# Kernel tuning notes

Hardware: AMD Instinct MI355X
Metric: run time of the kernel (lower is better)

## Reference

```python
import jax, jax.numpy as jnp
import numpy as np

KERNEL_MUL = 2.0
KERNEL_NUM = 5

N_S = 4096
N_T = 4096
D = 512
N_CLS = 10


def setup_inputs() -> dict:
    key = jax.random.key(0)
    k1, k2, k3 = jax.random.split(key, 3)
    x = jax.random.normal(k1, (N_S + N_T, D), dtype=jnp.float32)
    # source-first domain labels: first N_S are source (0), rest target (1)
    domain_labels = jnp.concatenate(
        [jnp.zeros((N_S,), dtype=jnp.int32), jnp.ones((N_T,), dtype=jnp.int32)]
    )
    y_true = jax.random.randint(k2, (N_S,), 0, N_CLS, dtype=jnp.int32)
    im_weights = jax.random.uniform(k3, (N_CLS,), dtype=jnp.float32, minval=0.5, maxval=1.5)
    return {
        "x": x,
        "im_weights": im_weights,
        "domain_labels": domain_labels,
        "y_true": y_true,
        "alpha": 1,
    }


def _gaussian_kernel_sum(total, n_samples):
    # Pairwise squared L2 distances via Gram trick instead of the O(N^2*D)
    # broadcasted tensor the torch code materializes (same math).
    sq = jnp.sum(total * total, axis=1)                      # [N]
    l2 = sq[:, None] + sq[None, :] - 2.0 * (total @ total.T)  # [N, N]
    l2 = jnp.maximum(l2, 0.0)
    # bandwidth computed on detached distances (torch uses L2_distance.data)
    bandwidth = jnp.sum(jax.lax.stop_gradient(l2)) / float(n_samples * n_samples - n_samples)
    bandwidth = bandwidth / (KERNEL_MUL ** (KERNEL_NUM // 2))
    k = jnp.zeros_like(l2)
    for i in range(KERNEL_NUM):
        k = k + jnp.exp(-l2 / (bandwidth * (KERNEL_MUL ** i)))
    return k


def reference(x, im_weights, domain_labels, y_true, alpha):
    dl = np.asarray(domain_labels)  # int labels are concrete constants
    src = np.where(dl == 0)[0]
    tgt = np.where(dl == 1)[0]
    n_s, n_t = len(src), len(tgt)

    total = jnp.concatenate([x[src], x[tgt]], axis=0)        # [n_s+n_t, D]
    kernels = _gaussian_kernel_sum(total, n_s + n_t)         # [N, N]

    # importance weights are detached in the torch code
    iw = jax.lax.stop_gradient(alpha * im_weights + (1.0 - alpha))
    w = iw[y_true]                                           # [n_s]

    k_ss = kernels[:n_s, :n_s]
    k_tt = kernels[n_s:, n_s:]
    k_st = kernels[:n_s, n_s:]

    # loss_1: weighted source upper-triangle + unweighted target upper-triangle
    loss_1 = jnp.sum(jnp.triu(k_ss * (w[:, None] * w[None, :]), k=1)) / float(n_s * (n_s - 1) / 2)
    loss_1 = loss_1 + jnp.sum(jnp.triu(k_tt, k=1)) / float(n_t * (n_t - 1) / 2)

    # loss_2: cross term, weighted by source sample weights
    loss_2 = jnp.sum(k_st * w[:, None]) / float(n_s * n_t)

    return loss_1 - 2.0 * loss_2
```

## Files before the change

### kernel.cpp

```cpp
#include <hip/hip_runtime.h>
#include <math.h>

#define N_TOT 8192
#define N_SRC 4096
#define D_DIM 512
#define BM2 256
#define NT2 (N_TOT / BM2)
#define NTILES2 (NT2 * (NT2 + 1) / 2)
#define NPREP 256

typedef short bf16x8 __attribute__((ext_vector_type(8)));
typedef unsigned short u16x8 __attribute__((ext_vector_type(8)));
typedef float f32x4 __attribute__((ext_vector_type(4)));


__device__ __forceinline__ unsigned short f2bf_rn(float v) {
    unsigned int u = __float_as_uint(v);
    unsigned int r = (u + 0x7FFFu + ((u >> 16) & 1u)) >> 16;
    return (unsigned short)r;
}

__global__ __launch_bounds__(256) void k_prep(const float* __restrict__ x,
                                              unsigned short* __restrict__ xhi,
                                              float* __restrict__ sq,
                                              float* __restrict__ colpart) {
    const int wave = threadIdx.x >> 6;
    const int lane = threadIdx.x & 63;
    __shared__ float colbuf[4][512];
    float fcol[8];
#pragma unroll
    for (int j = 0; j < 8; ++j) fcol[j] = 0.f;
#pragma unroll
    for (int r8 = 0; r8 < 8; ++r8) {
        const int row = blockIdx.x * 32 + wave * 8 + r8;
        const size_t base = (size_t)row * D_DIM + lane * 8;
        float v[8];
        *(float4*)&v[0] = *(const float4*)(x + base);
        *(float4*)&v[4] = *(const float4*)(x + base + 4);
        u16x8 h;
        float s = 0.f;
#pragma unroll
        for (int j = 0; j < 8; ++j) {
            h[j] = f2bf_rn(v[j]);
            s = fmaf(v[j], v[j], s);
            fcol[j] += v[j];
        }
        *(u16x8*)(xhi + base) = h;
#pragma unroll
        for (int off = 32; off; off >>= 1) s += __shfl_xor(s, off);
        if (lane == 0) sq[row] = s;
    }
#pragma unroll
    for (int j = 0; j < 8; ++j) colbuf[wave][lane * 8 + j] = fcol[j];
    __syncthreads();
    const int c = threadIdx.x * 2;
    float2 r;
    r.x = colbuf[0][c] + colbuf[1][c] + colbuf[2][c] + colbuf[3][c];
    r.y = colbuf[0][c + 1] + colbuf[1][c + 1] + colbuf[2][c + 1] + colbuf[3][c + 1];
    *(float2*)(colpart + (size_t)blockIdx.x * D_DIM + c) = r;
}

__global__ __launch_bounds__(256) void k_bw(const float* __restrict__ sq,
                                            const float* __restrict__ colpart,
                                            const float* __restrict__ imw,
                                            const int* __restrict__ y,
                                            const int* __restrict__ alpha_p,
                                            float* __restrict__ w,
                                            float* __restrict__ invbw,
                                            double* __restrict__ accum,
                                            unsigned int* __restrict__ cnt) {
    const int tid = threadIdx.x;
    if (tid == 0) { accum[2] = 0.0; *cnt = 0u; }
    const float a = (float)alpha_p[0];
    for (int i = tid; i < N_SRC; i += 256) w[i] = a * imw[y[i]] + (1.0f - a);
    double s2 = 0.0;
    for (int i = tid; i < N_TOT; i += 256) s2 += (double)sq[i];
    double cs0 = 0.0, cs1 = 0.0;
    const int c = tid * 2;
#pragma unroll 8
    for (int b = 0; b < NPREP; ++b) {
        float2 v = *(const float2*)(colpart + (size_t)b * D_DIM + c);
        cs0 += (double)v.x;
        cs1 += (double)v.y;
    }
    double sc = cs0 * cs0 + cs1 * cs1;
    __shared__ double r1[256], r2[256];
    r1[tid] = s2; r2[tid] = sc;
    __syncthreads();
    for (int off = 128; off; off >>= 1) {
        if (tid < off) { r1[tid] += r1[tid + off]; r2[tid] += r2[tid + off]; }
        __syncthreads();
    }
    if (tid == 0) {
        double sum_l2 = 2.0 * (double)N_TOT * r1[0] - 2.0 * sc * 0.0 - 2.0 * r2[0];
        double bw = sum_l2 / ((double)N_TOT * (double)N_TOT - (double)N_TOT);
        bw *= 0.25;
        double m = 1.0;
        for (int i = 0; i < 5; ++i) { invbw[i] = (float)(1.0 / (bw * m)); m *= 2.0; }
    }
}

__device__ __forceinline__ void gload_lds16(const unsigned short* g, char* l) {
    __builtin_amdgcn_global_load_lds((const __attribute__((address_space(1))) void*)g,
                                     (__attribute__((address_space(3))) void*)l,
                                     16, 0, 0);
}

__global__ __launch_bounds__(512, 2) void k_pairs(const unsigned short* __restrict__ xhi,
                                                  const float* __restrict__ sq,
                                                  const float* __restrict__ w,
                                                  const float* __restrict__ invbw,
                                                  double* __restrict__ accum,
                                                  unsigned int* __restrict__ cnt,
                                                  float* __restrict__ out) {
    int bid = (blockIdx.x & 7) * (NTILES2 / 8) + (blockIdx.x >> 3);
    int ti = 0, rem = bid;
    while (rem >= NT2 - ti) { rem -= NT2 - ti; ++ti; }
    const int tj = ti + rem;
    const int i0 = ti * BM2, j0 = tj * BM2;

    __shared__ __align__(16) char lds[2 * 65536];
    __shared__ double sdl8[8];

    const int tid = threadIdx.x;
    const int lane = tid & 63;
    const int wave = tid >> 6;
    const int wr = wave >> 2, wc = wave & 3;
    const int lr = lane & 15, lg = lane >> 4;

    const int aBase = wr * 16384 + lr * 128;
    const int bBase = 32768 + (wc >> 1) * 16384 + (wc & 1) * 8192 + lr * 128;
    int cxor16[2];
    cxor16[0] = ((lg ^ (lr & 7)) << 4);
    cxor16[1] = (((4 + lg) ^ (lr & 7)) << 4);

    const int srow = tid >> 3;
    const int sc = (tid & 7) ^ (srow & 7);
    const unsigned short* aPanel = xhi + (size_t)i0 * D_DIM;
    const unsigned short* bPanel = xhi + (size_t)j0 * D_DIM;

    f32x4 acc[8][4];
#pragma unroll
    for (int m = 0; m < 8; ++m)
#pragma unroll
        for (int n = 0; n < 4; ++n) acc[m][n] = f32x4{0.f, 0.f, 0.f, 0.f};

#define STAGE_HT(P, h, b, kt)                                                          \
    do {                                                                               \
        const unsigned short* _p = (P) ? bPanel : aPanel;                              \
        char* _dst = lds + (b) * 65536 + (P) * 32768 + (h) * 16384 + tid * 16;         \
        _Pragma("unroll") for (int _r = 0; _r < 2; ++_r) {                             \
            gload_lds16(_p + (size_t)((h) * 128 + _r * 64 + srow) * D_DIM +            \
                            (kt) * 64 + sc * 8,                                        \
                        _dst + _r * 8192);                                             \
        }                                                                              \
    } while (0)

    STAGE_HT(0, 0, 0, 0); STAGE_HT(1, 0, 0, 0); STAGE_HT(1, 1, 0, 0); STAGE_HT(0, 1, 0, 0);
    STAGE_HT(1, 0, 1, 1); STAGE_HT(0, 0, 1, 1);
    asm volatile("s_waitcnt vmcnt(4)" ::: "memory");
    __builtin_amdgcn_s_barrier();
    __builtin_amdgcn_sched_barrier(0);

    bf16x8 aR[4][2], bLo[2][2], bHi[2][2];

#define LD_A(Mq)                                                                       \
    _Pragma("unroll") for (int _m = 0; _m < 4; ++_m)                                   \
    _Pragma("unroll") for (int _k = 0; _k < 2; ++_k)                                   \
        aR[_m][_k] = *(const bf16x8*)(base + aBase + (Mq) * 8192 + _m * 2048 + cxor16[_k]);
#define LD_B(dstB, Nq)                                                                 \
    _Pragma("unroll") for (int _n = 0; _n < 2; ++_n)                                   \
    _Pragma("unroll") for (int _k = 0; _k < 2; ++_k)                                   \
        dstB[_n][_k] = *(const bf16x8*)(base + bBase + ((Nq) * 2 + _n) * 2048 + cxor16[_k]);
#define MFMA_Q(Mq, Nq, B)                                                              \
    __builtin_amdgcn_s_setprio(1);                                                     \
    _Pragma("unroll") for (int _m = 0; _m < 4; ++_m)                                   \
    _Pragma("unroll") for (int _n = 0; _n < 2; ++_n)                                   \
    _Pragma("unroll") for (int _k = 0; _k < 2; ++_k)                                   \
        acc[(Mq) * 4 + _m][(Nq) * 2 + _n] = __builtin_amdgcn_mfma_f32_16x16x32_bf16(   \
            aR[_m][_k], B[_n][_k], acc[(Mq) * 4 + _m][(Nq) * 2 + _n], 0, 0, 0);        \
    __builtin_amdgcn_s_setprio(0);
#define BAR1()                                                                         \
    __builtin_amdgcn_s_barrier();                                                      \
    asm volatile("s_waitcnt lgkmcnt(0)" ::: "memory");                                 \
    __builtin_amdgcn_sched_barrier(0);
#define BAR2()                                                                         \
    __builtin_amdgcn_s_barrier();                                                      \
    __builtin_amdgcn_sched_barrier(0);

    for (int t = 0; t < 8; ++t) {
        const char* base = lds + (t & 1) * 65536;
        const int bn = (t + 1) & 1;
        LD_A(0); LD_B(bLo, 0);
        if (t < 7) STAGE_HT(1, 1, bn, t + 1);
        BAR1(); MFMA_Q(0, 0, bLo); BAR2();
        LD_B(bHi, 1);
        if (t < 7) STAGE_HT(0, 1, bn, t + 1);
        BAR1(); MFMA_Q(0, 1, bHi); BAR2();
        LD_A(1);
        if (t < 6) STAGE_HT(1, 0, t & 1, t + 2);
        BAR1(); MFMA_Q(1, 1, bHi); BAR2();
        if (t < 6) STAGE_HT(0, 0, t & 1, t + 2);
        BAR1(); MFMA_Q(1, 0, bLo);
        if (t < 6) { asm volatile("s_waitcnt vmcnt(4)" ::: "memory"); }
        else if (t == 6) { asm volatile("s_waitcnt vmcnt(0)" ::: "memory"); }
        BAR2();
    }
#undef STAGE_HT
#undef LD_A
#undef LD_B
#undef MFMA_Q
#undef BAR1
#undef BAR2

    const float nib4 = -invbw[4];
    const bool diag = (ti == tj);
    const int region = (tj < NT2 / 2) ? 0 : ((ti >= NT2 / 2) ? 1 : 2);

    float sqj[4], wj[4];
#pragma unroll
    for (int n = 0; n < 4; ++n) {
        int jg = j0 + wc * 64 + n * 16 + lr;
        sqj[n] = sq[jg];
        wj[n] = (jg < N_SRC) ? w[jg] : 0.f;
    }
    float facc = 0.f;
#pragma unroll
    for (int m = 0; m < 8; ++m)
#pragma unroll
        for (int jj = 0; jj < 4; ++jj) {
            const int rg = wr * 128 + m * 16 + lg * 4 + jj;
            const int i = i0 + rg;
            const float sqi = sq[i];
            const float wi = (i < N_SRC) ? w[i] : 0.f;
#pragma unroll
            for (int n = 0; n < 4; ++n) {
                const int cg = wc * 64 + n * 16 + lr;
                if (diag && rg >= cg) continue;
                float l2 = fmaf(-2.f, acc[m][n][jj], sqi + sqj[n]);
                l2 = fmaxf(l2, 0.f);
                float tt = __expf(l2 * nib4);
                float t2 = tt * tt, t4 = t2 * t2, t8 = t4 * t4, t16 = t8 * t8;
                float k5 = tt + t2 + t4 + t8 + t16;
                float cf;
                if (region == 0)      cf = wi * wj[n];
                else if (region == 1) cf = 1.f;
                else                  cf = wi;
                facc = fmaf(k5, cf, facc);
            }
        }

#pragma unroll
    for (int off = 32; off; off >>= 1) facc += __shfl_xor(facc, off);
    if (lane == 0) sdl8[wave] = (double)facc;
    __syncthreads();
    if (tid == 0) {
        const double C_SS = 1.0 / 8386560.0;
        const double C_ST = 2.0 / 16777216.0;
        double s = 0.0;
#pragma unroll
        for (int q = 0; q < 8; ++q) s += sdl8[q];
        double scale = (region == 2) ? -C_ST : C_SS;
        atomicAdd(&accum[2], scale * s);
        __threadfence();
        unsigned int old = atomicAdd(cnt, 1u);
        if (old == NTILES2 - 1) {
            double v = atomicAdd(&accum[2], 0.0);
            out[0] = (float)v;
        }
    }
}

extern "C" void kernel_launch(void* const* d_in, const int* in_sizes, int n_in,
                              void* d_out, int out_size, void* d_ws, size_t ws_size,
                              hipStream_t stream) {
    const float* x    = (const float*)d_in[0];
    const float* imw  = (const float*)d_in[1];
    const int*   y    = (const int*)d_in[3];
    const int*   alph = (const int*)d_in[4];
    float* out = (float*)d_out;

    char* ws = (char*)d_ws;
    double*       accum   = (double*)ws;
    unsigned int* cnt     = (unsigned int*)(ws + 64);
    float*        invbw   = (float*)(ws + 128);
    float*        sq      = (float*)(ws + 4096);
    float*        wgt     = (float*)(ws + 36864);
    float*        colpart = (float*)(ws + 53248);
    unsigned short* xhi   = (unsigned short*)(ws + 577536);

    k_prep<<<NPREP, 256, 0, stream>>>(x, xhi, sq, colpart);
    k_bw<<<1, 256, 0, stream>>>(sq, colpart, imw, y, alph, wgt, invbw, accum, cnt);
    k_pairs<<<NTILES2, 512, 0, stream>>>(xhi, sq, wgt, invbw, accum, cnt, out);
}
```

Baseline: 188.6 us.

## Atomically reduce column sums and replace explicit LDS waits with raw barriers

k_prep now accumulates the column sums straight into a 512-entry double buffer with atomics. This replaces the per-block partial array that the single-block k_bw kernel had to reduce serially, and it adds a memset to the launch sequence. In k_pairs, the barrier macros lose their explicit lgkmcnt(0) waits and sched_barriers and become plain inline-asm s_barrier. The global-to-LDS staging calls are also moved ahead of the LDS register reads so the compiler has more freedom to overlap them. The risks are atomic contention on 512 addresses and correctness hazards if LDS reads are no longer waited for before the MFMAs or the next overwrite.

```diff
diff --git a/kernel.cpp b/kernel.cpp
--- a/kernel.cpp
+++ b/kernel.cpp
@@ -23,7 +23,7 @@
 __global__ __launch_bounds__(256) void k_prep(const float* __restrict__ x,
                                               unsigned short* __restrict__ xhi,
                                               float* __restrict__ sq,
-                                              float* __restrict__ colpart) {
+                                              double* __restrict__ colsum) {
     const int wave = threadIdx.x >> 6;
     const int lane = threadIdx.x & 63;
     __shared__ float colbuf[4][512];
@@ -54,14 +54,14 @@
     for (int j = 0; j < 8; ++j) colbuf[wave][lane * 8 + j] = fcol[j];
     __syncthreads();
     const int c = threadIdx.x * 2;
-    float2 r;
-    r.x = colbuf[0][c] + colbuf[1][c] + colbuf[2][c] + colbuf[3][c];
-    r.y = colbuf[0][c + 1] + colbuf[1][c + 1] + colbuf[2][c + 1] + colbuf[3][c + 1];
-    *(float2*)(colpart + (size_t)blockIdx.x * D_DIM + c) = r;
+    double s0 = (double)(colbuf[0][c] + colbuf[1][c]) + (double)(colbuf[2][c] + colbuf[3][c]);
+    double s1 = (double)(colbuf[0][c + 1] + colbuf[1][c + 1]) + (double)(colbuf[2][c + 1] + colbuf[3][c + 1]);
+    atomicAdd(&colsum[c], s0);
+    atomicAdd(&colsum[c + 1], s1);
 }
 
 __global__ __launch_bounds__(256) void k_bw(const float* __restrict__ sq,
-                                            const float* __restrict__ colpart,
+                                            const double* __restrict__ colsum,
                                             const float* __restrict__ imw,
                                             const int* __restrict__ y,
                                             const int* __restrict__ alpha_p,
@@ -75,15 +75,11 @@
     for (int i = tid; i < N_SRC; i += 256) w[i] = a * imw[y[i]] + (1.0f - a);
     double s2 = 0.0;
     for (int i = tid; i < N_TOT; i += 256) s2 += (double)sq[i];
-    double cs0 = 0.0, cs1 = 0.0;
-    const int c = tid * 2;
-#pragma unroll 8
-    for (int b = 0; b < NPREP; ++b) {
-        float2 v = *(const float2*)(colpart + (size_t)b * D_DIM + c);
-        cs0 += (double)v.x;
-        cs1 += (double)v.y;
-    }
-    double sc = cs0 * cs0 + cs1 * cs1;
+    double sc = 0.0;
+    for (int c = tid; c < D_DIM; c += 256) {
+        double v = colsum[c];
+        sc += v * v;
+    }
     __shared__ double r1[256], r2[256];
     r1[tid] = s2; r2[tid] = sc;
     __syncthreads();
@@ -92,7 +88,7 @@
         __syncthreads();
     }
     if (tid == 0) {
-        double sum_l2 = 2.0 * (double)N_TOT * r1[0] - 2.0 * sc * 0.0 - 2.0 * r2[0];
+        double sum_l2 = 2.0 * (double)N_TOT * r1[0] - 2.0 * r2[0];
         double bw = sum_l2 / ((double)N_TOT * (double)N_TOT - (double)N_TOT);
         bw *= 0.25;
         double m = 1.0;
@@ -158,9 +154,7 @@
 
     STAGE_HT(0, 0, 0, 0); STAGE_HT(1, 0, 0, 0); STAGE_HT(1, 1, 0, 0); STAGE_HT(0, 1, 0, 0);
     STAGE_HT(1, 0, 1, 1); STAGE_HT(0, 0, 1, 1);
-    asm volatile("s_waitcnt vmcnt(4)" ::: "memory");
-    __builtin_amdgcn_s_barrier();
-    __builtin_amdgcn_sched_barrier(0);
+    asm volatile("s_waitcnt vmcnt(4)\n\ts_barrier" ::: "memory");
 
     bf16x8 aR[4][2], bLo[2][2], bHi[2][2];
 
@@ -180,38 +174,31 @@
         acc[(Mq) * 4 + _m][(Nq) * 2 + _n] = __builtin_amdgcn_mfma_f32_16x16x32_bf16(   \
             aR[_m][_k], B[_n][_k], acc[(Mq) * 4 + _m][(Nq) * 2 + _n], 0, 0, 0);        \
     __builtin_amdgcn_s_setprio(0);
-#define BAR1()                                                                         \
-    __builtin_amdgcn_s_barrier();                                                      \
-    asm volatile("s_waitcnt lgkmcnt(0)" ::: "memory");                                 \
-    __builtin_amdgcn_sched_barrier(0);
-#define BAR2()                                                                         \
-    __builtin_amdgcn_s_barrier();                                                      \
-    __builtin_amdgcn_sched_barrier(0);
+#define BARRIER() asm volatile("s_barrier" ::: "memory")
 
     for (int t = 0; t < 8; ++t) {
         const char* base = lds + (t & 1) * 65536;
         const int bn = (t + 1) & 1;
+        if (t < 7) STAGE_HT(1, 1, bn, t + 1);
         LD_A(0); LD_B(bLo, 0);
-        if (t < 7) STAGE_HT(1, 1, bn, t + 1);
-        BAR1(); MFMA_Q(0, 0, bLo); BAR2();
+        BARRIER(); MFMA_Q(0, 0, bLo); BARRIER();
+        if (t < 7) STAGE_HT(0, 1, bn, t + 1);
         LD_B(bHi, 1);
-        if (t < 7) STAGE_HT(0, 1, bn, t + 1);
-        BAR1(); MFMA_Q(0, 1, bHi); BAR2();
+        BARRIER(); MFMA_Q(0, 1, bHi); BARRIER();
+        if (t < 6) STAGE_HT(1, 0, t & 1, t + 2);
         LD_A(1);
-        if (t < 6) STAGE_HT(1, 0, t & 1, t + 2);
-        BAR1(); MFMA_Q(1, 1, bHi); BAR2();
+        BARRIER(); MFMA_Q(1, 1, bHi); BARRIER();
         if (t < 6) STAGE_HT(0, 0, t & 1, t + 2);
-        BAR1(); MFMA_Q(1, 0, bLo);
+        BARRIER(); MFMA_Q(1, 0, bLo);
         if (t < 6) { asm volatile("s_waitcnt vmcnt(4)" ::: "memory"); }
         else if (t == 6) { asm volatile("s_waitcnt vmcnt(0)" ::: "memory"); }
-        BAR2();
+        BARRIER();
     }
 #undef STAGE_HT
 #undef LD_A
 #undef LD_B
 #undef MFMA_Q
-#undef BAR1
-#undef BAR2
+#undef BARRIER
 
     const float nib4 = -invbw[4];
     const bool diag = (ti == tj);
@@ -281,15 +268,16 @@
     float* out = (float*)d_out;
 
     char* ws = (char*)d_ws;
-    double*       accum   = (double*)ws;
-    unsigned int* cnt     = (unsigned int*)(ws + 64);
-    float*        invbw   = (float*)(ws + 128);
-    float*        sq      = (float*)(ws + 4096);
-    float*        wgt     = (float*)(ws + 36864);
-    float*        colpart = (float*)(ws + 53248);
-    unsigned short* xhi   = (unsigned short*)(ws + 577536);
-
-    k_prep<<<NPREP, 256, 0, stream>>>(x, xhi, sq, colpart);
-    k_bw<<<1, 256, 0, stream>>>(sq, colpart, imw, y, alph, wgt, invbw, accum, cnt);
+    double*       accum  = (double*)ws;
+    unsigned int* cnt    = (unsigned int*)(ws + 64);
+    float*        invbw  = (float*)(ws + 128);
+    double*       colsum = (double*)(ws + 4096);
+    float*        sq     = (float*)(ws + 8192);
+    float*        wgt    = (float*)(ws + 40960);
+    unsigned short* xhi  = (unsigned short*)(ws + 65536);
+
+    hipMemsetAsync(ws + 4096, 0, 4096, stream);
+    k_prep<<<NPREP, 256, 0, stream>>>(x, xhi, sq, colsum);
+    k_bw<<<1, 256, 0, stream>>>(sq, colsum, imw, y, alph, wgt, invbw, accum, cnt);
     k_pairs<<<NTILES2, 512, 0, stream>>>(xhi, sq, wgt, invbw, accum, cnt, out);
 }
```

Measured after the change: 186.8 us. Within noise of the previous version (-1.0%).
